# Optimization experiments

Measured on AMD Instinct MI355X. Metric: run time of the kernel, lower is better.

The kernel has to match this reference:

```python
import jax, jax.numpy as jnp
import numpy as np

THRESHOLD = 0.5
N_SEG = 5
NEG_INF = -1e30
EPS = 1e-12  # F.normalize eps


def setup_inputs() -> dict:
    key = jax.random.key(0)
    kx, kl = jax.random.split(key)
    B, D, L = 4096, 512, 80
    x = jax.random.normal(kx, (B, D), dtype=jnp.float32)
    labels = jax.random.randint(kl, (B, L), 0, 2, dtype=jnp.int32)
    return {"x": x, "labels": labels}


def reference(x, labels):
    B = x.shape[0]
    labels_f = labels.astype(jnp.float32)
    # pairwise Jaccard over multi-hot labels
    intersection = labels_f @ labels_f.T                      # [B, B]
    counts = labels_f.sum(axis=1, keepdims=True)              # [B, 1]
    union = counts + counts.T - intersection
    jaccard = intersection / union                            # [B, B]
    # cosine similarity (F.normalize with eps clamp)
    norm = jnp.maximum(jnp.linalg.norm(x, axis=1, keepdims=True), EPS)
    nx = x / norm
    sim = nx @ nx.T                                           # [B, B]
    # --- sample positive (uniform among jaccard > threshold), fixed key ---
    pos_mask = jaccard > THRESHOLD
    valid_mask = jnp.any(pos_mask, axis=1)                    # [B]
    logits = jnp.where(pos_mask, 0.0, NEG_INF)
    sampled = jax.random.categorical(jax.random.key(42), logits, axis=-1)
    pos_samples = jnp.where(valid_mask, sampled, 0)           # invalid rows -> 0
    # --- top-k negatives: jaccard strictly below the positive's jaccard ---
    pos_sim_j = jaccard[jnp.arange(B), pos_samples]           # [B]
    neg_mask = jaccard < pos_sim_j[:, None]
    neg_sims = jnp.where(neg_mask, jaccard, -jnp.inf)
    _, neg_samples = jax.lax.top_k(neg_sims, N_SEG)           # [B, N_SEG]
    # --- contrastive loss on cosine sims at sampled indices ---
    rel_pos = sim[jnp.arange(B), pos_samples]                 # [B]
    rel_neg = jnp.take_along_axis(sim, neg_samples, axis=1)   # [B, N_SEG]
    exp_pos = jnp.exp(rel_pos)
    sum_exp_neg = jnp.exp(rel_neg).sum(axis=1)
    loss = -jnp.log(exp_pos / (exp_pos + sum_exp_neg))
    vm = valid_mask.astype(x.dtype)
    return (loss * vm).sum() / vm.sum()
```

## Files before the change

kernel.cpp:

```cpp
#include <hip/hip_runtime.h>
#include <stdint.h>

#define B_ROWS 4096
#define DIMS   512
#define NLAB   80
#define HALF_ROWS 2048
#define HCNT   8388608u
#define CHUNK  1024
#define SEGCAP 512u
#define NBLK   2048

typedef unsigned long long u64;

__device__ __forceinline__ uint32_t rotl32(uint32_t x, uint32_t d) {
    return (x << d) | (x >> (32u - d));
}

__device__ __forceinline__ void tf2x32_key42(uint32_t c0, uint32_t c1,
                                             uint32_t& o0, uint32_t& o1) {
    const uint32_t ks0 = 0u;
    const uint32_t ks1 = 42u;
    const uint32_t ks2 = 0x1BD11BDAu ^ 0u ^ 42u;
    uint32_t x0 = c0 + ks0;
    uint32_t x1 = c1 + ks1;
#define TF_RND(r) { x0 += x1; x1 = rotl32(x1, (r)); x1 ^= x0; }
    TF_RND(13u) TF_RND(15u) TF_RND(26u) TF_RND(6u)
    x0 += ks1; x1 += ks2 + 1u;
    TF_RND(17u) TF_RND(29u) TF_RND(16u) TF_RND(24u)
    x0 += ks2; x1 += ks0 + 2u;
    TF_RND(13u) TF_RND(15u) TF_RND(26u) TF_RND(6u)
    x0 += ks0; x1 += ks1 + 3u;
    TF_RND(17u) TF_RND(29u) TF_RND(16u) TF_RND(24u)
    x0 += ks1; x1 += ks2 + 4u;
    TF_RND(13u) TF_RND(15u) TF_RND(26u) TF_RND(6u)
    x0 += ks2; x1 += ks0 + 5u;
#undef TF_RND
    o0 = x0; o1 = x1;
}

__device__ __forceinline__ u64 shflx64(u64 v, int m) {
    uint32_t lo = __shfl_xor((uint32_t)(v & 0xFFFFFFFFull), m, 64);
    uint32_t hi = __shfl_xor((uint32_t)(v >> 32), m, 64);
    return ((u64)hi << 32) | (u64)lo;
}

__device__ __forceinline__ uint32_t umx(uint32_t a, uint32_t b) { return a > b ? a : b; }
__device__ __forceinline__ uint32_t umn(uint32_t a, uint32_t b) { return a < b ? a : b; }

__device__ __forceinline__ uint32_t mbcnt64(u64 m) {
    uint32_t c = __builtin_amdgcn_mbcnt_lo((uint32_t)m, 0u);
    return __builtin_amdgcn_mbcnt_hi((uint32_t)(m >> 32), c);
}

__device__ __forceinline__ void ins5_u32(uint32_t* t, uint32_t k) {
    t[4] = umx(t[4], k);
    uint32_t hi, lo;
    hi = umx(t[3], t[4]); lo = umn(t[3], t[4]); t[3] = hi; t[4] = lo;
    hi = umx(t[2], t[3]); lo = umn(t[2], t[3]); t[2] = hi; t[3] = lo;
    hi = umx(t[1], t[2]); lo = umn(t[1], t[2]); t[1] = hi; t[2] = lo;
    hi = umx(t[0], t[1]); lo = umn(t[0], t[1]); t[0] = hi; t[1] = lo;
}

__device__ __forceinline__ void wave_top5_1(uint32_t* t, uint32_t* f) {
#pragma unroll
    for (int k = 0; k < 5; ++k) {
        uint32_t m = t[0];
#pragma unroll
        for (int s = 1; s < 64; s <<= 1) m = umx(m, __shfl_xor(m, s, 64));
        f[k] = m;
        if (t[0] == m) { t[0]=t[1]; t[1]=t[2]; t[2]=t[3]; t[3]=t[4]; t[4]=0u; }
    }
}

__device__ __forceinline__ uint32_t jkey19(uint32_t it, uint32_t u) {
    const uint32_t n = it << 19;
    float f = (float)it * __builtin_amdgcn_rcpf((float)u) * 524288.0f;
    uint32_t ak = (uint32_t)f;
    int r = (int)(n - ak * u);
    if (r < 0) { ak--; r += (int)u; }
    if (r >= (int)u) ak++;
    return ak + 1u;
}


__global__ __launch_bounds__(256) void prep_kernel(const float* __restrict__ x,
                                                   const int* __restrict__ labels,
                                                   uint4* __restrict__ pk,
                                                   float* __restrict__ norms) {
    const int tid = threadIdx.x;
    const int lane = tid & 63;
    const int row = blockIdx.x * 4 + (tid >> 6);
    const int* lr = labels + (size_t)row * NLAB;
    const int la = lr[lane];
    const int lb = (lane < 16) ? lr[64 + lane] : 0;
    const u64 b0 = __ballot(la != 0);
    const u64 b1 = __ballot(lb != 0);
    const uint32_t w2 = (uint32_t)b1 & 0xFFFFu;
    const uint32_t cnt = (uint32_t)__popcll(b0) + (uint32_t)__popc(w2);
    if (lane == 0) pk[row] = make_uint4((uint32_t)b0, (uint32_t)(b0 >> 32), w2, cnt);
    const float* xr = x + (size_t)row * DIMS;
    float ss = 0.f;
#pragma unroll
    for (int u = 0; u < 8; ++u) { float v = xr[lane + 64 * u]; ss += v * v; }
#pragma unroll
    for (int m = 1; m < 64; m <<= 1) ss += __shfl_xor(ss, m, 64);
    if (lane == 0) norms[row] = fmaxf(sqrtf(ss), 1e-12f);
}

__global__ __launch_bounds__(256) void fused_kernel(const float* __restrict__ x,
                                                    const uint4* __restrict__ pk,
                                                    const float* __restrict__ norms,
                                                    float2* __restrict__ blockPart) {
    __shared__ uint32_t segL[2][4][SEGCAP];
    __shared__ uint32_t cntL[2][4];
    __shared__ uint32_t tgL[2][6];
    __shared__ uint32_t validL[2];
    __shared__ float    simsL[2][6];
    __shared__ float    lossW[2], cntW2[2];

    const int tid = threadIdx.x;
    const int lane = tid & 63;
    const int sub  = tid >> 6;
    const int pr   = (int)blockIdx.x;
    const int r0 = pr, r1 = pr + HALF_ROWS;
    const uint4 P0 = pk[r0], P1 = pk[r1];
    const uint32_t cw0 = P0.w, cw1 = P1.w;
    const int jbase = sub * CHUNK;

    uint32_t cnt0 = 0u, cnt1 = 0u;
#pragma unroll 8
    for (int jb = 0; jb < CHUNK; jb += 64) {
        const int j = jbase + jb + lane;
        const uint4 pj = pk[j];
        const uint32_t cj = pj.w;
        const uint32_t it0 = (uint32_t)(__popc(P0.x & pj.x) + __popc(P0.y & pj.y) + __popc(P0.z & pj.z));
        const uint32_t u0  = cw0 + cj - it0;
        const uint32_t it1 = (uint32_t)(__popc(P1.x & pj.x) + __popc(P1.y & pj.y) + __popc(P1.z & pj.z));
        const uint32_t u1  = cw1 + cj - it1;
        const bool b0 = __umul24(it0, 20u) >= __umul24(u0, 9u);
        const bool b1 = __umul24(it1, 20u) >= __umul24(u1, 9u);
        const u64 bal0 = __ballot(b0);
        const u64 bal1 = __ballot(b1);
        if (b0) {
            const uint32_t off = cnt0 + mbcnt64(bal0);
            if (off < SEGCAP) segL[0][sub][off] = (it0 << 20) | (u0 << 12) | (uint32_t)j;
        }
        cnt0 += (uint32_t)__popcll(bal0);
        if (b1) {
            const uint32_t off = cnt1 + mbcnt64(bal1);
            if (off < SEGCAP) segL[1][sub][off] = (it1 << 20) | (u1 << 12) | (uint32_t)j;
        }
        cnt1 += (uint32_t)__popcll(bal1);
    }
    if (lane == 0) { cntL[0][sub] = cnt0; cntL[1][sub] = cnt1; }
    __syncthreads();

    if (sub < 2) {
        const int h = sub;
        uint32_t ns[4];
#pragma unroll
        for (int s = 0; s < 4; ++s) ns[s] = umn(cntL[h][s], SEGCAP);

        const uint32_t base23 = (uint32_t)pr * (uint32_t)B_ROWS;
        u64 gb = 0ull;
#pragma unroll
        for (int s = 0; s < 4; ++s) {
            for (int e = lane; e < (int)ns[s]; e += 64) {
                const uint32_t ent = segL[h][s][e];
                const uint32_t u  = (ent >> 12) & 0xFFu;
                const uint32_t it = ent >> 20;
                if ((it << 1) > u) {
                    const uint32_t j = ent & 0xFFFu;
                    uint32_t o0, o1;
                    tf2x32_key42(base23 + j, base23 + j + HCNT, o0, o1);
                    const uint32_t o = h ? o1 : o0;
                    const u64 key = ((u64)(o >> 9) << 41) | ((u64)((~j) & 0xFFFu) << 29) | (u64)jkey19(it, u);
                    if (key > gb) gb = key;
                }
            }
        }
#pragma unroll
        for (int m = 1; m < 64; m <<= 1) {
            const u64 o = shflx64(gb, m);
            if (o > gb) gb = o;
        }
        const bool valid = gb != 0ull;
        const int pos = valid ? (int)((~(uint32_t)(gb >> 29)) & 0xFFFu) : 0;
        const uint32_t pjkey = (uint32_t)(gb & 0xFFFFFu);

        uint32_t ts[5] = {0u, 0u, 0u, 0u, 0u};
#pragma unroll
        for (int s = 0; s < 4; ++s) {
            for (int e = lane; e < (int)ns[s]; e += 64) {
                const uint32_t ent = segL[h][s][e];
                const uint32_t j  = ent & 0xFFFu;
                const uint32_t u  = (ent >> 12) & 0xFFu;
                const uint32_t it = ent >> 20;
                const uint32_t k19 = jkey19(it, u);
                if (k19 < pjkey) ins5_u32(ts, (k19 << 12) | ((~j) & 0xFFFu));
            }
        }
        uint32_t tsf[5];
        wave_top5_1(ts, tsf);

        if (lane == 0) {
            tgL[h][0] = (uint32_t)pos;
#pragma unroll
            for (int k = 0; k < 5; ++k) tgL[h][k + 1] = (~tsf[k]) & 0xFFFu;
            validL[h] = valid ? 1u : 0u;
        }
    }
    __syncthreads();

#pragma unroll
    for (int k = 0; k < 3; ++k) {
        const int d = sub + 4 * k;
        const int h = (d >= 6) ? 1 : 0;
        const int q = d - 6 * h;
        const int row = h ? r1 : r0;
        const int tgt = (int)tgL[h][q];
        const float* pa = x + (size_t)row * DIMS;
        const float* pb = x + (size_t)tgt * DIMS;
        float s = 0.f;
#pragma unroll
        for (int u = 0; u < 8; ++u) s += pa[lane + 64 * u] * pb[lane + 64 * u];
#pragma unroll
        for (int m = 1; m < 64; m <<= 1) s += __shfl_xor(s, m, 64);
        if (lane == 0) simsL[h][q] = s;
    }
    __syncthreads();

    if (sub < 2 && lane == 0) {
        const int h = sub;
        float loss = 0.f, cnt = 0.f;
        if (validL[h]) {
            const int row = h ? r1 : r0;
            const float nr = norms[row];
            const float sp = simsL[h][0] / (nr * norms[tgL[h][0]]);
            float sen = 0.f;
#pragma unroll
            for (int q = 1; q < 6; ++q) sen += expf(simsL[h][q] / (nr * norms[tgL[h][q]]));
            const float ep = expf(sp);
            loss = -logf(ep / (ep + sen));
            cnt = 1.f;
        }
        lossW[h] = loss; cntW2[h] = cnt;
    }
    __syncthreads();
    if (tid == 0) blockPart[pr] = make_float2(lossW[0] + lossW[1], cntW2[0] + cntW2[1]);
}

__global__ __launch_bounds__(256) void final_kernel(const float2* __restrict__ blockPart,
                                                    float* __restrict__ out) {
    __shared__ float rl[4], rc[4];
    const int tid = threadIdx.x;
    const int lane = tid & 63;
    const int w = tid >> 6;
    float sl = 0.f, sc = 0.f;
#pragma unroll
    for (int k = 0; k < 8; ++k) {
        const float2 p = blockPart[tid + 256 * k];
        sl += p.x; sc += p.y;
    }
#pragma unroll
    for (int m = 1; m < 64; m <<= 1) {
        sl += __shfl_xor(sl, m, 64);
        sc += __shfl_xor(sc, m, 64);
    }
    if (lane == 0) { rl[w] = sl; rc[w] = sc; }
    __syncthreads();
    if (tid == 0) out[0] = (rl[0] + rl[1] + rl[2] + rl[3]) / (rc[0] + rc[1] + rc[2] + rc[3]);
}

extern "C" void kernel_launch(void* const* d_in, const int* in_sizes, int n_in,
                              void* d_out, int out_size, void* d_ws, size_t ws_size,
                              hipStream_t stream) {
    const float* x      = (const float*)d_in[0];
    const int*   labels = (const int*)d_in[1];
    float* out = (float*)d_out;

    char* ws = (char*)d_ws;
    uint4*  pk    = (uint4*)ws;
    float*  norms = (float*)(ws + 65536);
    float2* bPart = (float2*)(ws + 65536 + 16384);

    hipLaunchKernelGGL(prep_kernel,  dim3(1024), dim3(256), 0, stream, x, labels, pk, norms);
    hipLaunchKernelGGL(fused_kernel, dim3(2048), dim3(256), 0, stream, x, pk, norms, bPart);
    hipLaunchKernelGGL(final_kernel, dim3(1),    dim3(256), 0, stream, bPart, out);
}
```

Measured before the change: 88.39 us.

## Spread sampling and top-k across all four waves and fuse norms into fused kernel

The positive-sampling and negative top-5 phases now run on all four waves, each scanning its own segment, with cross-wave merges through shared memory, instead of leaving two waves idle. Row norms are no longer computed in the prep kernel. Each block computes its two row norms from registers preloaded before the Jaccard scan, and target norms are computed alongside the dot products. Target row loads are double-buffered. This removes the prep pass over x and balances the serial tail, at the cost of extra barriers, more registers and a branchless insert in the top-5 loop.

Measured after the change: 90.55 us. 1.02x slower.

```diff
diff --git a/kernel.cpp b/kernel.cpp
--- a/kernel.cpp
+++ b/kernel.cpp
@@ -61,6 +61,18 @@
     hi = umx(t[0], t[1]); lo = umn(t[0], t[1]); t[0] = hi; t[1] = lo;
 }
 
+__device__ __forceinline__ void merge5_u32(uint32_t* A, const uint32_t* Bv) {
+    uint32_t a0=A[0],a1=A[1],a2=A[2],a3=A[3],a4=A[4];
+    uint32_t b0=Bv[0],b1=Bv[1],b2=Bv[2],b3=Bv[3],b4=Bv[4];
+    uint32_t m0 = umx(a0, b0);
+    uint32_t m1 = umx(umx(a1, b1), umn(a0, b0));
+    uint32_t m2 = umx(umx(a2, b2), umx(umn(a0, b1), umn(a1, b0)));
+    uint32_t m3 = umx(umx(a3, b3), umx(umx(umn(a0, b2), umn(a1, b1)), umn(a2, b0)));
+    uint32_t m4 = umx(umx(a4, b4), umx(umx(umn(a0, b3), umn(a1, b2)),
+                                       umx(umn(a2, b1), umn(a3, b0))));
+    A[0]=m0; A[1]=m1; A[2]=m2; A[3]=m3; A[4]=m4;
+}
+
 __device__ __forceinline__ void wave_top5_1(uint32_t* t, uint32_t* f) {
 #pragma unroll
     for (int k = 0; k < 5; ++k) {
@@ -83,10 +95,8 @@
 }
 
 
-__global__ __launch_bounds__(256) void prep_kernel(const float* __restrict__ x,
-                                                   const int* __restrict__ labels,
-                                                   uint4* __restrict__ pk,
-                                                   float* __restrict__ norms) {
+__global__ __launch_bounds__(256) void prep_kernel(const int* __restrict__ labels,
+                                                   uint4* __restrict__ pk) {
     const int tid = threadIdx.x;
     const int lane = tid & 63;
     const int row = blockIdx.x * 4 + (tid >> 6);
@@ -98,24 +108,18 @@
     const uint32_t w2 = (uint32_t)b1 & 0xFFFFu;
     const uint32_t cnt = (uint32_t)__popcll(b0) + (uint32_t)__popc(w2);
     if (lane == 0) pk[row] = make_uint4((uint32_t)b0, (uint32_t)(b0 >> 32), w2, cnt);
-    const float* xr = x + (size_t)row * DIMS;
-    float ss = 0.f;
-#pragma unroll
-    for (int u = 0; u < 8; ++u) { float v = xr[lane + 64 * u]; ss += v * v; }
-#pragma unroll
-    for (int m = 1; m < 64; m <<= 1) ss += __shfl_xor(ss, m, 64);
-    if (lane == 0) norms[row] = fmaxf(sqrtf(ss), 1e-12f);
 }
 
 __global__ __launch_bounds__(256) void fused_kernel(const float* __restrict__ x,
                                                     const uint4* __restrict__ pk,
-                                                    const float* __restrict__ norms,
                                                     float2* __restrict__ blockPart) {
     __shared__ uint32_t segL[2][4][SEGCAP];
     __shared__ uint32_t cntL[2][4];
+    __shared__ u64      gpart[2][4];
+    __shared__ uint32_t keysL[2][4][5];
+    __shared__ uint32_t posL[2], pjkeyL[2], validL[2];
     __shared__ uint32_t tgL[2][6];
-    __shared__ uint32_t validL[2];
-    __shared__ float    simsL[2][6];
+    __shared__ float    simsL[2][6], normL[2][6], normR[2];
     __shared__ float    lossW[2], cntW2[2];
 
     const int tid = threadIdx.x;
@@ -126,6 +130,14 @@
     const uint4 P0 = pk[r0], P1 = pk[r1];
     const uint32_t cw0 = P0.w, cw1 = P1.w;
     const int jbase = sub * CHUNK;
+
+    float xa[8], xb[8];
+    {
+        const float* pa = x + (size_t)r0 * DIMS + lane;
+        const float* pb = x + (size_t)r1 * DIMS + lane;
+#pragma unroll
+        for (int u = 0; u < 8; ++u) { xa[u] = pa[64 * u]; xb[u] = pb[64 * u]; }
+    }
 
     uint32_t cnt0 = 0u, cnt1 = 0u;
 #pragma unroll 8
@@ -155,78 +167,139 @@
     if (lane == 0) { cntL[0][sub] = cnt0; cntL[1][sub] = cnt1; }
     __syncthreads();
 
-    if (sub < 2) {
-        const int h = sub;
-        uint32_t ns[4];
-#pragma unroll
-        for (int s = 0; s < 4; ++s) ns[s] = umn(cntL[h][s], SEGCAP);
-
-        const uint32_t base23 = (uint32_t)pr * (uint32_t)B_ROWS;
+    const uint32_t base23 = (uint32_t)pr * (uint32_t)B_ROWS;
+#pragma unroll
+    for (int h = 0; h < 2; ++h) {
+        const int n = (int)umn(cntL[h][sub], SEGCAP);
         u64 gb = 0ull;
-#pragma unroll
-        for (int s = 0; s < 4; ++s) {
-            for (int e = lane; e < (int)ns[s]; e += 64) {
-                const uint32_t ent = segL[h][s][e];
-                const uint32_t u  = (ent >> 12) & 0xFFu;
-                const uint32_t it = ent >> 20;
-                if ((it << 1) > u) {
-                    const uint32_t j = ent & 0xFFFu;
-                    uint32_t o0, o1;
-                    tf2x32_key42(base23 + j, base23 + j + HCNT, o0, o1);
-                    const uint32_t o = h ? o1 : o0;
-                    const u64 key = ((u64)(o >> 9) << 41) | ((u64)((~j) & 0xFFFu) << 29) | (u64)jkey19(it, u);
-                    if (key > gb) gb = key;
-                }
-            }
+#pragma unroll 2
+        for (int e = lane; e < n; e += 64) {
+            const uint32_t ent = segL[h][sub][e];
+            const uint32_t u  = (ent >> 12) & 0xFFu;
+            const uint32_t it = ent >> 20;
+            const uint32_t j  = ent & 0xFFFu;
+            uint32_t o0, o1;
+            tf2x32_key42(base23 + j, base23 + j + HCNT, o0, o1);
+            const uint32_t o = h ? o1 : o0;
+            const u64 key = ((u64)(o >> 9) << 41) | ((u64)((~j) & 0xFFFu) << 29) | (u64)jkey19(it, u);
+            if (((it << 1) > u) && key > gb) gb = key;
         }
 #pragma unroll
         for (int m = 1; m < 64; m <<= 1) {
             const u64 o = shflx64(gb, m);
             if (o > gb) gb = o;
         }
-        const bool valid = gb != 0ull;
-        const int pos = valid ? (int)((~(uint32_t)(gb >> 29)) & 0xFFFu) : 0;
-        const uint32_t pjkey = (uint32_t)(gb & 0xFFFFFu);
-
+        if (lane == 0) gpart[h][sub] = gb;
+    }
+    __syncthreads();
+
+    if (sub < 2 && lane < 4) {
+        const int h = sub;
+        u64 g = gpart[h][lane];
+        { const u64 o = shflx64(g, 1); if (o > g) g = o; }
+        { const u64 o = shflx64(g, 2); if (o > g) g = o; }
+        if (lane == 0) {
+            const bool valid = g != 0ull;
+            validL[h] = valid ? 1u : 0u;
+            posL[h]   = valid ? ((~(uint32_t)(g >> 29)) & 0xFFFu) : 0u;
+            pjkeyL[h] = (uint32_t)(g & 0xFFFFFu);
+        }
+    }
+    __syncthreads();
+
+#pragma unroll
+    for (int h = 0; h < 2; ++h) {
+        const int n = (int)umn(cntL[h][sub], SEGCAP);
+        const uint32_t pjkey = pjkeyL[h];
         uint32_t ts[5] = {0u, 0u, 0u, 0u, 0u};
-#pragma unroll
-        for (int s = 0; s < 4; ++s) {
-            for (int e = lane; e < (int)ns[s]; e += 64) {
-                const uint32_t ent = segL[h][s][e];
-                const uint32_t j  = ent & 0xFFFu;
-                const uint32_t u  = (ent >> 12) & 0xFFu;
-                const uint32_t it = ent >> 20;
-                const uint32_t k19 = jkey19(it, u);
-                if (k19 < pjkey) ins5_u32(ts, (k19 << 12) | ((~j) & 0xFFFu));
-            }
-        }
-        uint32_t tsf[5];
-        wave_top5_1(ts, tsf);
-
+#pragma unroll 2
+        for (int e = lane; e < n; e += 64) {
+            const uint32_t ent = segL[h][sub][e];
+            const uint32_t j  = ent & 0xFFFu;
+            const uint32_t u  = (ent >> 12) & 0xFFu;
+            const uint32_t it = ent >> 20;
+            const uint32_t k19 = jkey19(it, u);
+            const uint32_t key = (k19 < pjkey) ? ((k19 << 12) | ((~j) & 0xFFFu)) : 0u;
+            ins5_u32(ts, key);
+        }
+        uint32_t f[5];
+        wave_top5_1(ts, f);
         if (lane == 0) {
-            tgL[h][0] = (uint32_t)pos;
-#pragma unroll
-            for (int k = 0; k < 5; ++k) tgL[h][k + 1] = (~tsf[k]) & 0xFFFu;
-            validL[h] = valid ? 1u : 0u;
-        }
-    }
-    __syncthreads();
-
+#pragma unroll
+            for (int k = 0; k < 5; ++k) keysL[h][sub][k] = f[k];
+        }
+    }
+    __syncthreads();
+
+    if (sub < 2 && lane == 0) {
+        const int h = sub;
+        uint32_t f[5];
+#pragma unroll
+        for (int k = 0; k < 5; ++k) f[k] = keysL[h][0][k];
+#pragma unroll
+        for (int s = 1; s < 4; ++s) merge5_u32(f, keysL[h][s]);
+        tgL[h][0] = posL[h];
+#pragma unroll
+        for (int k = 0; k < 5; ++k) tgL[h][k + 1] = (~f[k]) & 0xFFFu;
+    }
+    __syncthreads();
+
+    if (sub < 2) {
+        float ss = 0.f;
+        if (sub == 0) {
+#pragma unroll
+            for (int u = 0; u < 8; ++u) ss += xa[u] * xa[u];
+        } else {
+#pragma unroll
+            for (int u = 0; u < 8; ++u) ss += xb[u] * xb[u];
+        }
+#pragma unroll
+        for (int m = 1; m < 64; m <<= 1) ss += __shfl_xor(ss, m, 64);
+        if (lane == 0) normR[sub] = fmaxf(sqrtf(ss), 1e-12f);
+    }
+
+    int hk[3], qk[3], tgt[3];
 #pragma unroll
     for (int k = 0; k < 3; ++k) {
         const int d = sub + 4 * k;
-        const int h = (d >= 6) ? 1 : 0;
-        const int q = d - 6 * h;
-        const int row = h ? r1 : r0;
-        const int tgt = (int)tgL[h][q];
-        const float* pa = x + (size_t)row * DIMS;
-        const float* pb = x + (size_t)tgt * DIMS;
-        float s = 0.f;
-#pragma unroll
-        for (int u = 0; u < 8; ++u) s += pa[lane + 64 * u] * pb[lane + 64 * u];
-#pragma unroll
-        for (int m = 1; m < 64; m <<= 1) s += __shfl_xor(s, m, 64);
-        if (lane == 0) simsL[h][q] = s;
+        hk[k] = (d >= 6) ? 1 : 0;
+        qk[k] = d - 6 * hk[k];
+        tgt[k] = (int)tgL[hk[k]][qk[k]];
+    }
+    float pv0[8], pv1[8];
+    {
+        const float* p = x + (size_t)tgt[0] * DIMS + lane;
+#pragma unroll
+        for (int u = 0; u < 8; ++u) pv0[u] = p[64 * u];
+    }
+#pragma unroll
+    for (int k = 0; k < 3; ++k) {
+        float* cur = (k & 1) ? pv1 : pv0;
+        float* nxt = (k & 1) ? pv0 : pv1;
+        if (k < 2) {
+            const float* p = x + (size_t)tgt[k + 1] * DIMS + lane;
+#pragma unroll
+            for (int u = 0; u < 8; ++u) nxt[u] = p[64 * u];
+        }
+        float s = 0.f, nb = 0.f;
+        if (hk[k]) {
+#pragma unroll
+            for (int u = 0; u < 8; ++u) s += xb[u] * cur[u];
+        } else {
+#pragma unroll
+            for (int u = 0; u < 8; ++u) s += xa[u] * cur[u];
+        }
+#pragma unroll
+        for (int u = 0; u < 8; ++u) nb += cur[u] * cur[u];
+#pragma unroll
+        for (int m = 1; m < 64; m <<= 1) {
+            s  += __shfl_xor(s, m, 64);
+            nb += __shfl_xor(nb, m, 64);
+        }
+        if (lane == 0) {
+            simsL[hk[k]][qk[k]] = s;
+            normL[hk[k]][qk[k]] = fmaxf(sqrtf(nb), 1e-12f);
+        }
     }
     __syncthreads();
 
@@ -234,12 +307,11 @@
         const int h = sub;
         float loss = 0.f, cnt = 0.f;
         if (validL[h]) {
-            const int row = h ? r1 : r0;
-            const float nr = norms[row];
-            const float sp = simsL[h][0] / (nr * norms[tgL[h][0]]);
+            const float nr = normR[h];
+            const float sp = simsL[h][0] / (nr * normL[h][0]);
             float sen = 0.f;
 #pragma unroll
-            for (int q = 1; q < 6; ++q) sen += expf(simsL[h][q] / (nr * norms[tgL[h][q]]));
+            for (int q = 1; q < 6; ++q) sen += expf(simsL[h][q] / (nr * normL[h][q]));
             const float ep = expf(sp);
             loss = -logf(ep / (ep + sen));
             cnt = 1.f;
@@ -281,10 +353,9 @@
 
     char* ws = (char*)d_ws;
     uint4*  pk    = (uint4*)ws;
-    float*  norms = (float*)(ws + 65536);
-    float2* bPart = (float2*)(ws + 65536 + 16384);
-
-    hipLaunchKernelGGL(prep_kernel,  dim3(1024), dim3(256), 0, stream, x, labels, pk, norms);
-    hipLaunchKernelGGL(fused_kernel, dim3(2048), dim3(256), 0, stream, x, pk, norms, bPart);
+    float2* bPart = (float2*)(ws + 65536);
+
+    hipLaunchKernelGGL(prep_kernel,  dim3(1024), dim3(256), 0, stream, labels, pk);
+    hipLaunchKernelGGL(fused_kernel, dim3(NBLK), dim3(256), 0, stream, x, pk, bPart);
     hipLaunchKernelGGL(final_kernel, dim3(1),    dim3(256), 0, stream, bPart, out);
 }
```

## Spread positive-sampling and top-5 negative selection across all four waves

Applied to the files above, without the earlier changes.

Previously only two of the four waves did the positive sampling and top-5 scan, each walking all four segment lists of its row. Now every wave scans its own segment for both rows. Per-wave partial maxima and top-5 lists go to shared memory and are combined with a sorted 5-way merge. The top-5 insert is made branchless and both rows share one shuffle reduction. This adds two more barriers and a serial merge on lane 0 in exchange for spreading the scan over all waves.

Result: no change. 87.40 us (-1.1%).

```diff
diff --git a/kernel.cpp b/kernel.cpp
--- a/kernel.cpp
+++ b/kernel.cpp
@@ -61,14 +61,31 @@
     hi = umx(t[0], t[1]); lo = umn(t[0], t[1]); t[0] = hi; t[1] = lo;
 }
 
-__device__ __forceinline__ void wave_top5_1(uint32_t* t, uint32_t* f) {
+__device__ __forceinline__ void merge5_u32(uint32_t* A, const uint32_t* Bv) {
+    uint32_t a0=A[0],a1=A[1],a2=A[2],a3=A[3],a4=A[4];
+    uint32_t b0=Bv[0],b1=Bv[1],b2=Bv[2],b3=Bv[3],b4=Bv[4];
+    uint32_t m0 = umx(a0, b0);
+    uint32_t m1 = umx(umx(a1, b1), umn(a0, b0));
+    uint32_t m2 = umx(umx(a2, b2), umx(umn(a0, b1), umn(a1, b0)));
+    uint32_t m3 = umx(umx(a3, b3), umx(umx(umn(a0, b2), umn(a1, b1)), umn(a2, b0)));
+    uint32_t m4 = umx(umx(a4, b4), umx(umx(umn(a0, b3), umn(a1, b2)),
+                                       umx(umn(a2, b1), umn(a3, b0))));
+    A[0]=m0; A[1]=m1; A[2]=m2; A[3]=m3; A[4]=m4;
+}
+
+__device__ __forceinline__ void wave_top5_2(uint32_t* ta, uint32_t* tb,
+                                            uint32_t* fa, uint32_t* fb) {
 #pragma unroll
     for (int k = 0; k < 5; ++k) {
-        uint32_t m = t[0];
-#pragma unroll
-        for (int s = 1; s < 64; s <<= 1) m = umx(m, __shfl_xor(m, s, 64));
-        f[k] = m;
-        if (t[0] == m) { t[0]=t[1]; t[1]=t[2]; t[2]=t[3]; t[3]=t[4]; t[4]=0u; }
+        uint32_t ma = ta[0], mb = tb[0];
+#pragma unroll
+        for (int s = 1; s < 64; s <<= 1) {
+            ma = umx(ma, __shfl_xor(ma, s, 64));
+            mb = umx(mb, __shfl_xor(mb, s, 64));
+        }
+        fa[k] = ma; fb[k] = mb;
+        if (ta[0] == ma) { ta[0]=ta[1]; ta[1]=ta[2]; ta[2]=ta[3]; ta[3]=ta[4]; ta[4]=0u; }
+        if (tb[0] == mb) { tb[0]=tb[1]; tb[1]=tb[2]; tb[2]=tb[3]; tb[3]=tb[4]; tb[4]=0u; }
     }
 }
 
@@ -113,8 +130,10 @@
                                                     float2* __restrict__ blockPart) {
     __shared__ uint32_t segL[2][4][SEGCAP];
     __shared__ uint32_t cntL[2][4];
+    __shared__ u64      gpart[2][4];
+    __shared__ uint32_t keysL[2][4][5];
+    __shared__ uint32_t posL[2], pjkeyL[2], validL[2];
     __shared__ uint32_t tgL[2][6];
-    __shared__ uint32_t validL[2];
     __shared__ float    simsL[2][6];
     __shared__ float    lossW[2], cntW2[2];
 
@@ -155,28 +174,22 @@
     if (lane == 0) { cntL[0][sub] = cnt0; cntL[1][sub] = cnt1; }
     __syncthreads();
 
-    if (sub < 2) {
-        const int h = sub;
-        uint32_t ns[4];
-#pragma unroll
-        for (int s = 0; s < 4; ++s) ns[s] = umn(cntL[h][s], SEGCAP);
-
-        const uint32_t base23 = (uint32_t)pr * (uint32_t)B_ROWS;
+    const uint32_t base23 = (uint32_t)pr * (uint32_t)B_ROWS;
+#pragma unroll
+    for (int h = 0; h < 2; ++h) {
+        const int n = (int)umn(cntL[h][sub], SEGCAP);
         u64 gb = 0ull;
-#pragma unroll
-        for (int s = 0; s < 4; ++s) {
-            for (int e = lane; e < (int)ns[s]; e += 64) {
-                const uint32_t ent = segL[h][s][e];
-                const uint32_t u  = (ent >> 12) & 0xFFu;
-                const uint32_t it = ent >> 20;
-                if ((it << 1) > u) {
-                    const uint32_t j = ent & 0xFFFu;
-                    uint32_t o0, o1;
-                    tf2x32_key42(base23 + j, base23 + j + HCNT, o0, o1);
-                    const uint32_t o = h ? o1 : o0;
-                    const u64 key = ((u64)(o >> 9) << 41) | ((u64)((~j) & 0xFFFu) << 29) | (u64)jkey19(it, u);
-                    if (key > gb) gb = key;
-                }
+        for (int e = lane; e < n; e += 64) {
+            const uint32_t ent = segL[h][sub][e];
+            const uint32_t u  = (ent >> 12) & 0xFFu;
+            const uint32_t it = ent >> 20;
+            if ((it << 1) > u) {
+                const uint32_t j = ent & 0xFFFu;
+                uint32_t o0, o1;
+                tf2x32_key42(base23 + j, base23 + j + HCNT, o0, o1);
+                const uint32_t o = h ? o1 : o0;
+                const u64 key = ((u64)(o >> 9) << 41) | ((u64)((~j) & 0xFFFu) << 29) | (u64)jkey19(it, u);
+                if (key > gb) gb = key;
             }
         }
 #pragma unroll
@@ -184,31 +197,65 @@
             const u64 o = shflx64(gb, m);
             if (o > gb) gb = o;
         }
-        const bool valid = gb != 0ull;
-        const int pos = valid ? (int)((~(uint32_t)(gb >> 29)) & 0xFFFu) : 0;
-        const uint32_t pjkey = (uint32_t)(gb & 0xFFFFFu);
-
-        uint32_t ts[5] = {0u, 0u, 0u, 0u, 0u};
-#pragma unroll
-        for (int s = 0; s < 4; ++s) {
-            for (int e = lane; e < (int)ns[s]; e += 64) {
-                const uint32_t ent = segL[h][s][e];
-                const uint32_t j  = ent & 0xFFFu;
-                const uint32_t u  = (ent >> 12) & 0xFFu;
-                const uint32_t it = ent >> 20;
-                const uint32_t k19 = jkey19(it, u);
-                if (k19 < pjkey) ins5_u32(ts, (k19 << 12) | ((~j) & 0xFFFu));
-            }
-        }
-        uint32_t tsf[5];
-        wave_top5_1(ts, tsf);
-
+        if (lane == 0) gpart[h][sub] = gb;
+    }
+    __syncthreads();
+
+    if (sub < 2 && lane == 0) {
+        const int h = sub;
+        u64 g = gpart[h][0];
+        if (gpart[h][1] > g) g = gpart[h][1];
+        if (gpart[h][2] > g) g = gpart[h][2];
+        if (gpart[h][3] > g) g = gpart[h][3];
+        const bool valid = g != 0ull;
+        validL[h] = valid ? 1u : 0u;
+        posL[h]   = valid ? ((~(uint32_t)(g >> 29)) & 0xFFFu) : 0u;
+        pjkeyL[h] = (uint32_t)(g & 0xFFFFFu);
+    }
+    __syncthreads();
+
+    {
+        const uint32_t pj0 = pjkeyL[0], pj1 = pjkeyL[1];
+        const int n0 = (int)umn(cntL[0][sub], SEGCAP);
+        const int n1 = (int)umn(cntL[1][sub], SEGCAP);
+        uint32_t t0[5] = {0u,0u,0u,0u,0u}, t1[5] = {0u,0u,0u,0u,0u};
+        for (int e = lane; e < n0; e += 64) {
+            const uint32_t ent = segL[0][sub][e];
+            const uint32_t j  = ent & 0xFFFu;
+            const uint32_t u  = (ent >> 12) & 0xFFu;
+            const uint32_t it = ent >> 20;
+            const uint32_t k19 = jkey19(it, u);
+            const uint32_t key = (k19 < pj0) ? ((k19 << 12) | ((~j) & 0xFFFu)) : 0u;
+            ins5_u32(t0, key);
+        }
+        for (int e = lane; e < n1; e += 64) {
+            const uint32_t ent = segL[1][sub][e];
+            const uint32_t j  = ent & 0xFFFu;
+            const uint32_t u  = (ent >> 12) & 0xFFu;
+            const uint32_t it = ent >> 20;
+            const uint32_t k19 = jkey19(it, u);
+            const uint32_t key = (k19 < pj1) ? ((k19 << 12) | ((~j) & 0xFFFu)) : 0u;
+            ins5_u32(t1, key);
+        }
+        uint32_t f0[5], f1[5];
+        wave_top5_2(t0, t1, f0, f1);
         if (lane == 0) {
-            tgL[h][0] = (uint32_t)pos;
-#pragma unroll
-            for (int k = 0; k < 5; ++k) tgL[h][k + 1] = (~tsf[k]) & 0xFFFu;
-            validL[h] = valid ? 1u : 0u;
-        }
+#pragma unroll
+            for (int k = 0; k < 5; ++k) { keysL[0][sub][k] = f0[k]; keysL[1][sub][k] = f1[k]; }
+        }
+    }
+    __syncthreads();
+
+    if (sub < 2 && lane == 0) {
+        const int h = sub;
+        uint32_t f[5];
+#pragma unroll
+        for (int k = 0; k < 5; ++k) f[k] = keysL[h][0][k];
+#pragma unroll
+        for (int s = 1; s < 4; ++s) merge5_u32(f, keysL[h][s]);
+        tgL[h][0] = posL[h];
+#pragma unroll
+        for (int k = 0; k < 5; ++k) tgL[h][k + 1] = (~f[k]) & 0xFFFu;
     }
     __syncthreads();
 
@@ -285,6 +332,6 @@
     float2* bPart = (float2*)(ws + 65536 + 16384);
 
     hipLaunchKernelGGL(prep_kernel,  dim3(1024), dim3(256), 0, stream, x, labels, pk, norms);
-    hipLaunchKernelGGL(fused_kernel, dim3(2048), dim3(256), 0, stream, x, pk, norms, bPart);
+    hipLaunchKernelGGL(fused_kernel, dim3(NBLK), dim3(256), 0, stream, x, pk, norms, bPart);
     hipLaunchKernelGGL(final_kernel, dim3(1),    dim3(256), 0, stream, bPart, out);
 }
```
